# Kernel tuning notes

Hardware: AMD Instinct MI355X
Metric: run time of the kernel (lower is better)

The kernel has to match this reference:

```python
import jax, jax.numpy as jnp
import numpy as np

NEG_SLOPE = 0.2


def _gat(x, src, dst, W, a_src, a_dst, b, N):
    # PyG GATConv (eval mode, concat=True). W: [Fin, H*C], a_*: [H, C], b: [H*C]
    H, C = a_src.shape
    h = (x @ W).reshape(N, H, C)                       # [N,H,C]
    al_s = jnp.einsum('nhc,hc->nh', h, a_src)          # source attention logits
    al_d = jnp.einsum('nhc,hc->nh', h, a_dst)          # target attention logits
    e = jax.nn.leaky_relu(al_s[src] + al_d[dst], NEG_SLOPE)  # [E,H]
    m = jax.ops.segment_max(e, dst, num_segments=N)
    m = jnp.where(jnp.isneginf(m), 0.0, m)
    p = jnp.exp(e - m[dst])
    s = jax.ops.segment_sum(p, dst, num_segments=N)
    alpha = p / (s[dst] + 1e-16)                       # segment softmax over incoming edges
    out = jax.ops.segment_sum(h[src] * alpha[:, :, None], dst, num_segments=N)
    return out.reshape(N, H * C) + b


def _lin(key, fin, fout):
    k1, k2 = jax.random.split(key)
    w = jax.random.normal(k1, (fin, fout), jnp.float32) / np.sqrt(fin)
    b = jax.random.normal(k2, (fout,), jnp.float32) * 0.01
    return w, b


def _gat_params(key, fin, H, C):
    k1, k2, k3, k4 = jax.random.split(key, 4)
    W = jax.random.normal(k1, (fin, H * C), jnp.float32) / np.sqrt(fin)
    a_s = jax.random.normal(k2, (H, C), jnp.float32) / np.sqrt(C)
    a_d = jax.random.normal(k3, (H, C), jnp.float32) / np.sqrt(C)
    b = jax.random.normal(k4, (H * C,), jnp.float32) * 0.01
    return W, a_s, a_d, b


def setup_inputs() -> dict:
    key = jax.random.key(0)
    N, E, F, HID, H = 20000, 320000, 128, 128, 2
    W_ = HID * H  # 256
    ks = jax.random.split(key, 12)
    x = jax.random.normal(ks[0], (N, F), jnp.float32)
    edge_index = jax.random.randint(ks[1], (2, E), 0, N, jnp.int64)
    edge_attr = jax.random.normal(ks[2], (E, 4), jnp.float32)
    ec_w1, ec_b1 = _lin(ks[3], 2 * F, HID)
    ec_w2, ec_b2 = _lin(ks[4], HID, HID)
    g1 = _gat_params(ks[5], HID, H, HID)
    g2 = _gat_params(ks[6], W_, H, HID)
    reg_w, reg_b = _lin(ks[7], W_, W_)
    g3 = _gat_params(ks[8], W_, H, HID)
    g4 = _gat_params(ks[9], W_, H, HID)
    fin_w, fin_b = _lin(ks[10], W_, 1)
    d = {"x": x, "edge_index": edge_index, "edge_attr": edge_attr,
         "ec_w1": ec_w1, "ec_b1": ec_b1, "ec_w2": ec_w2, "ec_b2": ec_b2,
         "reg_w": reg_w, "reg_b": reg_b, "fin_w": fin_w, "fin_b": fin_b}
    for name, p in (("g1", g1), ("g2", g2), ("g3", g3), ("g4", g4)):
        d[name + "_w"], d[name + "_as"], d[name + "_ad"], d[name + "_b"] = p
    return d


def reference(x, edge_index, edge_attr,
              ec_w1, ec_b1, ec_w2, ec_b2,
              g1_w, g1_as, g1_ad, g1_b,
              g2_w, g2_as, g2_ad, g2_b,
              reg_w, reg_b,
              g3_w, g3_as, g3_ad, g3_b,
              g4_w, g4_as, g4_ad, g4_b,
              fin_w, fin_b):
    N = x.shape[0]
    src, dst = edge_index[0], edge_index[1]
    # EdgeConv: msg = MLP([x_i, x_j - x_i]), max-aggregation at target i (no self loops)
    xi = x[dst]
    msg = jnp.concatenate([xi, x[src] - xi], axis=-1)          # [E, 2F]
    h = jnp.maximum(msg @ ec_w1 + ec_b1, 0.0) @ ec_w2 + ec_b2   # [E, HID]
    agg = jax.ops.segment_max(h, dst, num_segments=N)
    x = jnp.where(jnp.isneginf(agg), 0.0, agg)
    # GATConv adds self loops by default
    loop = jnp.arange(N, dtype=src.dtype)
    s2 = jnp.concatenate([src, loop])
    d2 = jnp.concatenate([dst, loop])
    # edge_attr is ignored by GATConv (edge_dim=None)
    x = jax.nn.relu(_gat(x, s2, d2, g1_w, g1_as, g1_ad, g1_b, N))
    r = x
    x = jax.nn.relu(_gat(x, s2, d2, g2_w, g2_as, g2_ad, g2_b, N)) + r
    x = x @ reg_w + reg_b
    r = x
    x = jax.nn.relu(_gat(x, s2, d2, g3_w, g3_as, g3_ad, g3_b, N)) + r
    x = jax.nn.relu(_gat(x, s2, d2, g4_w, g4_as, g4_ad, g4_b, N))
    return x @ fin_w + fin_b
```

## Files before the change

kernel.cpp:

```cpp
#include <hip/hip_runtime.h>
#include <math.h>


#define NEG_SLOPE 0.2f

typedef short short8 __attribute__((ext_vector_type(8)));
typedef float float4v __attribute__((ext_vector_type(4)));

__device__ __forceinline__ float leaky(float x) { return x > 0.f ? x : NEG_SLOPE * x; }

__device__ __forceinline__ void atomicMaxF(float* addr, float v) {
  if (v >= 0.f) atomicMax((int*)addr, __float_as_int(v));
  else          atomicMin((unsigned int*)addr, __float_as_uint(v));
}

__device__ __forceinline__ unsigned short bf16_rn(float f) {
  unsigned u = __float_as_uint(f);
  unsigned r = (u + 0x7FFFu + ((u >> 16) & 1u)) >> 16;
  return (unsigned short)r;
}
__device__ __forceinline__ float bf16_to_f(unsigned short h) {
  return __uint_as_float(((unsigned)h) << 16);
}

__global__ __launch_bounds__(256) void k_fill_f32(float* p, float v, int n) {
  int i = blockIdx.x * 256 + threadIdx.x;
  if (i < n) p[i] = v;
}

__global__ __launch_bounds__(256) void k_hist(const int* __restrict__ ei, int* __restrict__ deg,
                                              int E) {
  int e = blockIdx.x * 256 + threadIdx.x;
  if (e < E) atomicAdd(&deg[ei[E + e]], 1);
}

__global__ __launch_bounds__(1024) void k_scan(const int* __restrict__ deg, int* __restrict__ rs,
                                               int n) {
  __shared__ int wsum[16];
  __shared__ int carry;
  int tid = threadIdx.x, lane = tid & 63, wv = tid >> 6;
  if (tid == 0) carry = 0;
  __syncthreads();
  for (int base = 0; base < n; base += 1024) {
    int i = base + tid;
    int v = (i < n) ? deg[i] : 0;
    int s = v;
    #pragma unroll
    for (int o = 1; o < 64; o <<= 1) {
      int t = __shfl(s, lane - o);
      if (lane >= o) s += t;
    }
    if (lane == 63) wsum[wv] = s;
    __syncthreads();
    if (wv == 0) {
      int x = (lane < 16) ? wsum[lane] : 0;
      #pragma unroll
      for (int o = 1; o < 16; o <<= 1) {
        int t = __shfl(x, lane - o);
        if (lane >= o) x += t;
      }
      if (lane < 16) wsum[lane] = x;
    }
    __syncthreads();
    int woff = carry + (wv ? wsum[wv - 1] : 0);
    if (i < n) rs[i] = woff + s - v;
    __syncthreads();
    if (tid == 0) carry += wsum[15];
    __syncthreads();
  }
  if (tid == 0) rs[n] = carry;
}

__global__ __launch_bounds__(256) void k_scatter(const int* __restrict__ ei,
                                                 const int* __restrict__ rs,
                                                 int* __restrict__ cnt,
                                                 int* __restrict__ csr_src,
                                                 int* __restrict__ csr_dst, int E) {
  int e = blockIdx.x * 256 + threadIdx.x;
  if (e < E) {
    int d = ei[E + e];
    int p = atomicAdd(&cnt[d], 1);
    int slot = rs[d] + p;
    csr_src[slot] = ei[e];
    csr_dst[slot] = d;
  }
}

struct SplitJob {
  const float* W;
  const float* aux;
  unsigned short* Th;
  unsigned short* Tl;
  float* bias_out;
  int K, N, kshift, type;
};
struct SplitJobs { SplitJob j[7]; };

__global__ __launch_bounds__(256) void k_prep_all(SplitJobs jobs) {
  SplitJob jb = jobs.j[blockIdx.y];
  int idx = blockIdx.x * 256 + threadIdx.x;
  if (idx >= jb.K * jb.N) return;
  float v;
  if (jb.type == 0) {
    int n = idx >> jb.kshift;
    int k = idx & (jb.K - 1);
    v = jb.W[k * jb.N + n];
  } else {
    int n = idx >> 7;
    int k = idx & 127;
    if (n < 128) v = jb.W[k * 128 + n] - jb.W[(k + 128) * 128 + n];
    else         v = jb.W[(k + 128) * 128 + (n - 128)];
    if (idx < 256) jb.bias_out[idx] = (idx < 128) ? jb.aux[idx] : 0.f;
  }
  unsigned short h = bf16_rn(v);
  jb.Th[idx] = h;
  jb.Tl[idx] = bf16_rn(v - bf16_to_f(h));
}

__global__ __launch_bounds__(256) void k_gemm_mfma(const float* __restrict__ A,
                                                   const unsigned short* __restrict__ BTh,
                                                   const unsigned short* __restrict__ BTl,
                                                   const float* __restrict__ bias,
                                                   float* __restrict__ C, int M, int K,
                                                   const float* __restrict__ a_s,
                                                   const float* __restrict__ a_d,
                                                   float* __restrict__ al_out) {
  __shared__ __align__(16) unsigned short Ash[64][40];
  __shared__ __align__(16) unsigned short Asl[64][40];
  __shared__ __align__(16) unsigned short Bsh[128][40];
  __shared__ __align__(16) unsigned short Bsl[128][40];
  __shared__ float alS[64][2];
  const int tid = threadIdx.x;
  const int bm = blockIdx.x * 64;
  const int bn = blockIdx.y * 128;
  const int w = tid >> 6, lane = tid & 63, quad = lane >> 4, lr = lane & 15;
  float4v zero4 = {0.f, 0.f, 0.f, 0.f};
  float4v acc[4][2];
  #pragma unroll
  for (int mt = 0; mt < 4; ++mt)
    #pragma unroll
    for (int nt = 0; nt < 2; ++nt) acc[mt][nt] = zero4;

  const int arow = tid >> 2;
  const int akq = (tid & 3) * 8;
  const int agr = bm + arow;

  #pragma unroll 4
  for (int k0 = 0; k0 < K; k0 += 32) {
    float av[8];
    if (agr < M) {
      float4 a0 = *(const float4*)&A[(size_t)agr * K + k0 + akq];
      float4 a1 = *(const float4*)&A[(size_t)agr * K + k0 + akq + 4];
      av[0] = a0.x; av[1] = a0.y; av[2] = a0.z; av[3] = a0.w;
      av[4] = a1.x; av[5] = a1.y; av[6] = a1.z; av[7] = a1.w;
    } else {
      #pragma unroll
      for (int i = 0; i < 8; ++i) av[i] = 0.f;
    }
    short8 h8, l8;
    #pragma unroll
    for (int i = 0; i < 8; ++i) {
      unsigned short h = bf16_rn(av[i]);
      h8[i] = (short)h;
      l8[i] = (short)bf16_rn(av[i] - bf16_to_f(h));
    }
    *(short8*)&Ash[arow][akq] = h8;
    *(short8*)&Asl[arow][akq] = l8;
    #pragma unroll
    for (int c = tid; c < 512; c += 256) {
      int n = c >> 2, kq2 = (c & 3) * 8;
      *(short8*)&Bsh[n][kq2] = *(const short8*)&BTh[(size_t)(bn + n) * K + k0 + kq2];
      *(short8*)&Bsl[n][kq2] = *(const short8*)&BTl[(size_t)(bn + n) * K + k0 + kq2];
    }
    __syncthreads();
    short8 ah[4], alo[4], bh[2], blo[2];
    #pragma unroll
    for (int mt = 0; mt < 4; ++mt) {
      ah[mt]  = *(short8*)&Ash[mt * 16 + lr][quad * 8];
      alo[mt] = *(short8*)&Asl[mt * 16 + lr][quad * 8];
    }
    #pragma unroll
    for (int nt = 0; nt < 2; ++nt) {
      bh[nt]  = *(short8*)&Bsh[w * 32 + nt * 16 + lr][quad * 8];
      blo[nt] = *(short8*)&Bsl[w * 32 + nt * 16 + lr][quad * 8];
    }
    #pragma unroll
    for (int mt = 0; mt < 4; ++mt)
      #pragma unroll
      for (int nt = 0; nt < 2; ++nt) {
        acc[mt][nt] = __builtin_amdgcn_mfma_f32_16x16x32_bf16(ah[mt], bh[nt], acc[mt][nt], 0, 0, 0);
        acc[mt][nt] = __builtin_amdgcn_mfma_f32_16x16x32_bf16(alo[mt], bh[nt], acc[mt][nt], 0, 0, 0);
        acc[mt][nt] = __builtin_amdgcn_mfma_f32_16x16x32_bf16(ah[mt], blo[nt], acc[mt][nt], 0, 0, 0);
      }
    __syncthreads();
  }
  #pragma unroll
  for (int nt = 0; nt < 2; ++nt) {
    int n = bn + w * 32 + nt * 16 + lr;
    float bv = bias ? bias[n] : 0.f;
    #pragma unroll
    for (int mt = 0; mt < 4; ++mt) {
      #pragma unroll
      for (int r = 0; r < 4; ++r) {
        int m = bm + mt * 16 + quad * 4 + r;
        if (m < M) C[(size_t)m * 256 + n] = acc[mt][nt][r] + bv;
      }
    }
  }
  if (a_s) {
    if (tid < 128) ((float*)alS)[tid] = 0.f;
    __syncthreads();
    float asv[2], adv[2];
    #pragma unroll
    for (int nt = 0; nt < 2; ++nt) {
      int n = bn + w * 32 + nt * 16 + lr;
      asv[nt] = a_s[n];
      adv[nt] = a_d[n];
    }
    #pragma unroll
    for (int mt = 0; mt < 4; ++mt) {
      #pragma unroll
      for (int r = 0; r < 4; ++r) {
        float ps = acc[mt][0][r] * asv[0] + acc[mt][1][r] * asv[1];
        float pd = acc[mt][0][r] * adv[0] + acc[mt][1][r] * adv[1];
        #pragma unroll
        for (int o = 8; o; o >>= 1) {
          ps += __shfl_xor(ps, o);
          pd += __shfl_xor(pd, o);
        }
        if (lr == 0) {
          int row = mt * 16 + quad * 4 + r;
          atomicAdd(&alS[row][0], ps);
          atomicAdd(&alS[row][1], pd);
        }
      }
    }
    __syncthreads();
    int head = bn >> 7;
    if (tid < 64) {
      int m = bm + tid;
      if (m < M) {
        al_out[m * 4 + head]     = alS[tid][0];
        al_out[m * 4 + 2 + head] = alS[tid][1];
      }
    }
  }
}

__global__ __launch_bounds__(256, 4) void k_edgeconv2(const float* __restrict__ uv,
                                                      const int* __restrict__ csr_src,
                                                      const int* __restrict__ csr_dst,
                                                      const unsigned short* __restrict__ w2Th,
                                                      const unsigned short* __restrict__ w2Tl,
                                                      const float* __restrict__ b2,
                                                      float* __restrict__ x0, int E) {
  __shared__ __align__(16) char smem[34816];
  unsigned short (*Ph)[136] = (unsigned short(*)[136])smem;
  unsigned short (*Pl)[136] = (unsigned short(*)[136])(smem + 17408);
  float (*H2)[132] = (float(*)[132])smem;
  __shared__ int sSrc[64], sDst[64];

  const int tid = threadIdx.x;
  const int e0 = blockIdx.x * 64;
  const int w = tid >> 6, lane = tid & 63, quad = lane >> 4, lr = lane & 15;
  if (tid < 64) {
    int e = e0 + tid;
    sSrc[tid] = (e < E) ? csr_src[e] : -1;
    sDst[tid] = (e < E) ? csr_dst[e] : -1;
  }
  __syncthreads();
  #pragma unroll
  for (int c = tid; c < 1024; c += 256) {
    int r = c >> 4;
    int kq = (c & 15) * 8;
    float pv[8];
    int sn = sSrc[r], dn = sDst[r];
    if (sn >= 0) {
      float4 u0 = *(const float4*)&uv[(size_t)dn * 256 + kq];
      float4 u1 = *(const float4*)&uv[(size_t)dn * 256 + kq + 4];
      float4 v0 = *(const float4*)&uv[(size_t)sn * 256 + 128 + kq];
      float4 v1 = *(const float4*)&uv[(size_t)sn * 256 + 128 + kq + 4];
      pv[0] = fmaxf(u0.x + v0.x, 0.f); pv[1] = fmaxf(u0.y + v0.y, 0.f);
      pv[2] = fmaxf(u0.z + v0.z, 0.f); pv[3] = fmaxf(u0.w + v0.w, 0.f);
      pv[4] = fmaxf(u1.x + v1.x, 0.f); pv[5] = fmaxf(u1.y + v1.y, 0.f);
      pv[6] = fmaxf(u1.z + v1.z, 0.f); pv[7] = fmaxf(u1.w + v1.w, 0.f);
    } else {
      #pragma unroll
      for (int i = 0; i < 8; ++i) pv[i] = 0.f;
    }
    short8 h8, l8;
    #pragma unroll
    for (int i = 0; i < 8; ++i) {
      unsigned short h = bf16_rn(pv[i]);
      h8[i] = (short)h;
      l8[i] = (short)bf16_rn(pv[i] - bf16_to_f(h));
    }
    *(short8*)&Ph[r][kq] = h8;
    *(short8*)&Pl[r][kq] = l8;
  }
  __syncthreads();
  float4v zero4 = {0.f, 0.f, 0.f, 0.f};
  float4v acc[4][2];
  #pragma unroll
  for (int mt = 0; mt < 4; ++mt)
    #pragma unroll
    for (int nt = 0; nt < 2; ++nt) acc[mt][nt] = zero4;

  #pragma unroll
  for (int k0 = 0; k0 < 128; k0 += 32) {
    short8 ah[4], alo[4], bh[2], blo[2];
    #pragma unroll
    for (int nt = 0; nt < 2; ++nt) {
      int n = w * 32 + nt * 16 + lr;
      bh[nt]  = *(const short8*)&w2Th[(size_t)n * 128 + k0 + quad * 8];
      blo[nt] = *(const short8*)&w2Tl[(size_t)n * 128 + k0 + quad * 8];
    }
    #pragma unroll
    for (int mt = 0; mt < 4; ++mt) {
      ah[mt]  = *(short8*)&Ph[mt * 16 + lr][k0 + quad * 8];
      alo[mt] = *(short8*)&Pl[mt * 16 + lr][k0 + quad * 8];
    }
    #pragma unroll
    for (int mt = 0; mt < 4; ++mt)
      #pragma unroll
      for (int nt = 0; nt < 2; ++nt) {
        acc[mt][nt] = __builtin_amdgcn_mfma_f32_16x16x32_bf16(ah[mt], bh[nt], acc[mt][nt], 0, 0, 0);
        acc[mt][nt] = __builtin_amdgcn_mfma_f32_16x16x32_bf16(alo[mt], bh[nt], acc[mt][nt], 0, 0, 0);
        acc[mt][nt] = __builtin_amdgcn_mfma_f32_16x16x32_bf16(ah[mt], blo[nt], acc[mt][nt], 0, 0, 0);
      }
  }
  __syncthreads();
  #pragma unroll
  for (int nt = 0; nt < 2; ++nt) {
    int n = w * 32 + nt * 16 + lr;
    float bv = b2[n];
    #pragma unroll
    for (int mt = 0; mt < 4; ++mt) {
      #pragma unroll
      for (int r = 0; r < 4; ++r) {
        int row = mt * 16 + quad * 4 + r;
        H2[row][n] = acc[mt][nt][r] + bv;
      }
    }
  }
  __syncthreads();
  if (tid < 128) {
    int col = tid;
    int prev = sDst[0];
    float rmax = H2[0][col];
    for (int r = 1; r < 64; ++r) {
      int d = sDst[r];
      float v = H2[r][col];
      if (d == prev) {
        rmax = fmaxf(rmax, v);
      } else {
        if (prev >= 0) atomicMaxF(&x0[(size_t)prev * 128 + col], rmax);
        prev = d;
        rmax = v;
      }
    }
    if (prev >= 0) atomicMaxF(&x0[(size_t)prev * 128 + col], rmax);
  }
}

__global__ __launch_bounds__(256) void k_finalize(float* p, int n) {
  int i = blockIdx.x * 256 + threadIdx.x;
  if (i < n) {
    float v = p[i];
    if (v == -INFINITY) p[i] = 0.f;
  }
}

__global__ __launch_bounds__(256) void k_gat_agg(const float* __restrict__ Hf,
                                                 const float* __restrict__ al,
                                                 const int* __restrict__ rs,
                                                 const int* __restrict__ csr_src,
                                                 const float* __restrict__ bias,
                                                 const float* __restrict__ res,
                                                 float* __restrict__ out, int N) {
  int wave = threadIdx.x >> 6, lane = threadIdx.x & 63;
  int i = blockIdx.x * 4 + wave;
  if (i >= N) return;
  int beg = rs[i], end = rs[i + 1];
  int deg = end - beg;
  float4 me = *(const float4*)&al[i * 4];
  float ad0 = me.z, ad1 = me.w;
  float sl0 = leaky(me.x + ad0);
  float sl1 = leaky(me.y + ad1);
  const int c = lane << 2;
  const int hsel = lane >> 5;
  float a0, a1, a2, a3;

  if (deg <= 64) {
    int s = 0;
    float l0 = -INFINITY, l1 = -INFINITY;
    bool act = lane < deg;
    if (act) {
      s = csr_src[beg + lane];
      float4 a4 = *(const float4*)&al[s * 4];
      l0 = leaky(a4.x + ad0);
      l1 = leaky(a4.y + ad1);
    }
    float m0 = fmaxf(sl0, l0), m1 = fmaxf(sl1, l1);
    #pragma unroll
    for (int o = 32; o; o >>= 1) {
      m0 = fmaxf(m0, __shfl_xor(m0, o));
      m1 = fmaxf(m1, __shfl_xor(m1, o));
    }
    float w0 = act ? __expf(l0 - m0) : 0.f;
    float w1 = act ? __expf(l1 - m1) : 0.f;
    float s0 = w0, s1 = w1;
    #pragma unroll
    for (int o = 32; o; o >>= 1) {
      s0 += __shfl_xor(s0, o);
      s1 += __shfl_xor(s1, o);
    }
    s0 += __expf(sl0 - m0);
    s1 += __expf(sl1 - m1);
    float inv0 = 1.f / (s0 + 1e-16f), inv1 = 1.f / (s1 + 1e-16f);
    float wp0 = w0 * inv0, wp1 = w1 * inv1;
    float wself = hsel ? __expf(sl1 - m1) * inv1 : __expf(sl0 - m0) * inv0;
    float4 hv = *(const float4*)&Hf[(size_t)i * 256 + c];
    a0 = wself * hv.x; a1 = wself * hv.y; a2 = wself * hv.z; a3 = wself * hv.w;
    float b0 = 0.f, b1 = 0.f, b2 = 0.f, b3 = 0.f;
    float c0 = 0.f, c1 = 0.f, c2 = 0.f, c3 = 0.f;
    float d0 = 0.f, d1 = 0.f, d2 = 0.f, d3 = 0.f;
    int j = 0;
    for (; j + 4 <= deg; j += 4) {
      int s_0 = __shfl(s, j);     float wA0 = __shfl(wp0, j);     float wB0 = __shfl(wp1, j);
      int s_1 = __shfl(s, j + 1); float wA1 = __shfl(wp0, j + 1); float wB1 = __shfl(wp1, j + 1);
      int s_2 = __shfl(s, j + 2); float wA2 = __shfl(wp0, j + 2); float wB2 = __shfl(wp1, j + 2);
      int s_3 = __shfl(s, j + 3); float wA3 = __shfl(wp0, j + 3); float wB3 = __shfl(wp1, j + 3);
      float4 h0 = *(const float4*)&Hf[(size_t)s_0 * 256 + c];
      float4 h1 = *(const float4*)&Hf[(size_t)s_1 * 256 + c];
      float4 h2 = *(const float4*)&Hf[(size_t)s_2 * 256 + c];
      float4 h3 = *(const float4*)&Hf[(size_t)s_3 * 256 + c];
      float w_0 = hsel ? wB0 : wA0;
      float w_1 = hsel ? wB1 : wA1;
      float w_2 = hsel ? wB2 : wA2;
      float w_3 = hsel ? wB3 : wA3;
      a0 += w_0 * h0.x; a1 += w_0 * h0.y; a2 += w_0 * h0.z; a3 += w_0 * h0.w;
      b0 += w_1 * h1.x; b1 += w_1 * h1.y; b2 += w_1 * h1.z; b3 += w_1 * h1.w;
      c0 += w_2 * h2.x; c1 += w_2 * h2.y; c2 += w_2 * h2.z; c3 += w_2 * h2.w;
      d0 += w_3 * h3.x; d1 += w_3 * h3.y; d2 += w_3 * h3.z; d3 += w_3 * h3.w;
    }
    for (; j < deg; ++j) {
      int sj = __shfl(s, j);
      float wA = __shfl(wp0, j), wB = __shfl(wp1, j);
      float wj = hsel ? wB : wA;
      float4 h4 = *(const float4*)&Hf[(size_t)sj * 256 + c];
      a0 += wj * h4.x; a1 += wj * h4.y; a2 += wj * h4.z; a3 += wj * h4.w;
    }
    a0 += b0 + c0 + d0; a1 += b1 + c1 + d1;
    a2 += b2 + c2 + d2; a3 += b3 + c3 + d3;
  } else {
    float m0 = sl0, m1 = sl1;
    for (int e = beg + lane; e < end; e += 64) {
      int s = csr_src[e];
      m0 = fmaxf(m0, leaky(al[s * 4 + 0] + ad0));
      m1 = fmaxf(m1, leaky(al[s * 4 + 1] + ad1));
    }
    #pragma unroll
    for (int o = 32; o; o >>= 1) {
      m0 = fmaxf(m0, __shfl_xor(m0, o));
      m1 = fmaxf(m1, __shfl_xor(m1, o));
    }
    float s0 = 0.f, s1 = 0.f;
    for (int e = beg + lane; e < end; e += 64) {
      int s = csr_src[e];
      s0 += __expf(leaky(al[s * 4 + 0] + ad0) - m0);
      s1 += __expf(leaky(al[s * 4 + 1] + ad1) - m1);
    }
    #pragma unroll
    for (int o = 32; o; o >>= 1) {
      s0 += __shfl_xor(s0, o);
      s1 += __shfl_xor(s1, o);
    }
    s0 += __expf(sl0 - m0);
    s1 += __expf(sl1 - m1);
    float inv0 = 1.f / (s0 + 1e-16f), inv1 = 1.f / (s1 + 1e-16f);
    float mh = hsel ? m1 : m0;
    float invh = hsel ? inv1 : inv0;
    float adh = hsel ? ad1 : ad0;
    float wself = __expf((hsel ? sl1 : sl0) - mh) * invh;
    float4 hv = *(const float4*)&Hf[(size_t)i * 256 + c];
    a0 = wself * hv.x; a1 = wself * hv.y; a2 = wself * hv.z; a3 = wself * hv.w;
    for (int e = beg; e < end; ++e) {
      int s = csr_src[e];
      float wgt = __expf(leaky(al[s * 4 + hsel] + adh) - mh) * invh;
      float4 h4 = *(const float4*)&Hf[(size_t)s * 256 + c];
      a0 += wgt * h4.x; a1 += wgt * h4.y; a2 += wgt * h4.z; a3 += wgt * h4.w;
    }
  }
  float4 bv = *(const float4*)&bias[c];
  float4 o4;
  o4.x = fmaxf(a0 + bv.x, 0.f);
  o4.y = fmaxf(a1 + bv.y, 0.f);
  o4.z = fmaxf(a2 + bv.z, 0.f);
  o4.w = fmaxf(a3 + bv.w, 0.f);
  if (res) {
    float4 r4 = *(const float4*)&res[(size_t)i * 256 + c];
    o4.x += r4.x; o4.y += r4.y; o4.z += r4.z; o4.w += r4.w;
  }
  *(float4*)&out[(size_t)i * 256 + c] = o4;
}

__global__ __launch_bounds__(256) void k_findot(const float* __restrict__ X,
                                                const float* __restrict__ fw,
                                                const float* __restrict__ fb,
                                                float* __restrict__ out, int N) {
  int wave = threadIdx.x >> 6, lane = threadIdx.x & 63;
  int i = blockIdx.x * 4 + wave;
  if (i >= N) return;
  float4 xv = *(const float4*)&X[(size_t)i * 256 + (lane << 2)];
  float4 wv = *(const float4*)&fw[lane << 2];
  float p = xv.x * wv.x + xv.y * wv.y + xv.z * wv.z + xv.w * wv.w;
  #pragma unroll
  for (int o = 32; o; o >>= 1) p += __shfl_xor(p, o);
  if (lane == 0) out[i] = p + fb[0];
}

extern "C" void kernel_launch(void* const* d_in, const int* in_sizes, int n_in,
                              void* d_out, int out_size, void* d_ws, size_t ws_size,
                              hipStream_t stream) {
  const float* x      = (const float*)d_in[0];
  const int*   ei     = (const int*)d_in[1];
  const float* ec_w1  = (const float*)d_in[3];
  const float* ec_b1  = (const float*)d_in[4];
  const float* ec_w2  = (const float*)d_in[5];
  const float* ec_b2  = (const float*)d_in[6];
  const float* reg_w  = (const float*)d_in[7];
  const float* reg_b  = (const float*)d_in[8];
  const float* fin_w  = (const float*)d_in[9];
  const float* fin_b  = (const float*)d_in[10];
  const float* g1_w   = (const float*)d_in[11];
  const float* g1_as  = (const float*)d_in[12];
  const float* g1_ad  = (const float*)d_in[13];
  const float* g1_b   = (const float*)d_in[14];
  const float* g2_w   = (const float*)d_in[15];
  const float* g2_as  = (const float*)d_in[16];
  const float* g2_ad  = (const float*)d_in[17];
  const float* g2_b   = (const float*)d_in[18];
  const float* g3_w   = (const float*)d_in[19];
  const float* g3_as  = (const float*)d_in[20];
  const float* g3_ad  = (const float*)d_in[21];
  const float* g3_b   = (const float*)d_in[22];
  const float* g4_w   = (const float*)d_in[23];
  const float* g4_as  = (const float*)d_in[24];
  const float* g4_ad  = (const float*)d_in[25];
  const float* g4_b   = (const float*)d_in[26];

  const int N = in_sizes[0] / 128;
  const int E = in_sizes[1] / 2;

  char* base = (char*)d_ws;
  size_t off = 0;
  auto alloc = [&](size_t bytes) -> char* {
    char* p = base + off;
    off += (bytes + 255) & ~(size_t)255;
    return p;
  };
  const size_t szN4 = ((size_t)N * 4 + 255) & ~(size_t)255;
  int*   deg      = (int*)alloc((size_t)N * 4);
  int*   cnt      = (int*)alloc((size_t)N * 4);
  int*   rs       = (int*)alloc((size_t)(N + 1) * 4);
  int*   csr_src  = (int*)alloc((size_t)E * 4);
  int*   csr_dst  = (int*)alloc((size_t)E * 4);
  float* bias_cat = (float*)alloc(256 * 4);
  unsigned short* bcatTh = (unsigned short*)alloc(256 * 128 * 2);
  unsigned short* bcatTl = (unsigned short*)alloc(256 * 128 * 2);
  unsigned short* w2Th   = (unsigned short*)alloc(128 * 128 * 2);
  unsigned short* w2Tl   = (unsigned short*)alloc(128 * 128 * 2);
  unsigned short* g1Th   = (unsigned short*)alloc(256 * 128 * 2);
  unsigned short* g1Tl   = (unsigned short*)alloc(256 * 128 * 2);
  unsigned short* g2Th   = (unsigned short*)alloc(256 * 256 * 2);
  unsigned short* g2Tl   = (unsigned short*)alloc(256 * 256 * 2);
  unsigned short* g3Th   = (unsigned short*)alloc(256 * 256 * 2);
  unsigned short* g3Tl   = (unsigned short*)alloc(256 * 256 * 2);
  unsigned short* g4Th   = (unsigned short*)alloc(256 * 256 * 2);
  unsigned short* g4Tl   = (unsigned short*)alloc(256 * 256 * 2);
  unsigned short* regTh  = (unsigned short*)alloc(256 * 256 * 2);
  unsigned short* regTl  = (unsigned short*)alloc(256 * 256 * 2);
  float* uv = (float*)alloc((size_t)N * 256 * 4);
  float* x0 = (float*)alloc((size_t)N * 128 * 4);
  float* X1 = (float*)alloc((size_t)N * 256 * 4);
  float* X2 = (float*)alloc((size_t)N * 256 * 4);
  float* al = (float*)alloc((size_t)N * 4 * 4);
  (void)ws_size; (void)n_in; (void)out_size;

  const int nodeWaveBlocks = (N + 3) / 4;
  const dim3 gemmGrid((N + 63) / 64, 2);

  SplitJobs jobs;
  jobs.j[0] = {ec_w2, nullptr, w2Th, w2Tl, nullptr, 128, 128, 7, 0};
  jobs.j[1] = {g1_w,  nullptr, g1Th, g1Tl, nullptr, 128, 256, 7, 0};
  jobs.j[2] = {g2_w,  nullptr, g2Th, g2Tl, nullptr, 256, 256, 8, 0};
  jobs.j[3] = {g3_w,  nullptr, g3Th, g3Tl, nullptr, 256, 256, 8, 0};
  jobs.j[4] = {g4_w,  nullptr, g4Th, g4Tl, nullptr, 256, 256, 8, 0};
  jobs.j[5] = {reg_w, nullptr, regTh, regTl, nullptr, 256, 256, 8, 0};
  jobs.j[6] = {ec_w1, ec_b1, bcatTh, bcatTl, bias_cat, 128, 256, 7, 1};
  k_prep_all<<<dim3(256, 7), 256, 0, stream>>>(jobs);

  hipMemsetAsync(deg, 0, 2 * szN4, stream);
  k_hist<<<(E + 255) / 256, 256, 0, stream>>>(ei, deg, E);
  k_scan<<<1, 1024, 0, stream>>>(deg, rs, N);
  k_scatter<<<(E + 255) / 256, 256, 0, stream>>>(ei, rs, cnt, csr_src, csr_dst, E);

  k_gemm_mfma<<<gemmGrid, 256, 0, stream>>>(x, bcatTh, bcatTl, bias_cat, uv, N, 128,
                                            nullptr, nullptr, nullptr);
  k_fill_f32<<<(N * 128 + 255) / 256, 256, 0, stream>>>(x0, -INFINITY, N * 128);
  k_edgeconv2<<<(E + 63) / 64, 256, 0, stream>>>(uv, csr_src, csr_dst, w2Th, w2Tl, ec_b2, x0, E);
  k_finalize<<<(N * 128 + 255) / 256, 256, 0, stream>>>(x0, N * 128);

  k_gemm_mfma<<<gemmGrid, 256, 0, stream>>>(x0, g1Th, g1Tl, nullptr, uv, N, 128,
                                            g1_as, g1_ad, al);
  k_gat_agg<<<nodeWaveBlocks, 256, 0, stream>>>(uv, al, rs, csr_src, g1_b, nullptr, X1, N);

  k_gemm_mfma<<<gemmGrid, 256, 0, stream>>>(X1, g2Th, g2Tl, nullptr, uv, N, 256,
                                            g2_as, g2_ad, al);
  k_gat_agg<<<nodeWaveBlocks, 256, 0, stream>>>(uv, al, rs, csr_src, g2_b, X1, X2, N);

  k_gemm_mfma<<<gemmGrid, 256, 0, stream>>>(X2, regTh, regTl, reg_b, X1, N, 256,
                                            nullptr, nullptr, nullptr);

  k_gemm_mfma<<<gemmGrid, 256, 0, stream>>>(X1, g3Th, g3Tl, nullptr, uv, N, 256,
                                            g3_as, g3_ad, al);
  k_gat_agg<<<nodeWaveBlocks, 256, 0, stream>>>(uv, al, rs, csr_src, g3_b, X1, X2, N);

  k_gemm_mfma<<<gemmGrid, 256, 0, stream>>>(X2, g4Th, g4Tl, nullptr, uv, N, 256,
                                            g4_as, g4_ad, al);
  k_gat_agg<<<nodeWaveBlocks, 256, 0, stream>>>(uv, al, rs, csr_src, g4_b, nullptr, X1, N);

  k_findot<<<nodeWaveBlocks, 256, 0, stream>>>(X1, fin_w, fin_b, (float*)d_out, N);
}
```

Baseline: 588.9 us.

## Pre-split activations to bf16 hi/lo in producers and drop GEMM LDS staging

Activations are now converted to bf16 high/low pairs once, in the producing kernel: the GAT aggregation epilogue, the GEMM epilogue, or a new split kernel. The -inf cleanup is folded into that split kernel, so the separate finalize launch goes away. The MFMA GEMM now loads A and B fragments straight from global memory, with no shared-memory staging and no barriers. This removes the per-tile fp32-to-bf16 split work and the synchronisation. In exchange, the four waves of a block load the same A rows redundantly and with less coalescing, and producers write extra hi/lo buffers.

```diff
diff --git a/kernel.cpp b/kernel.cpp
--- a/kernel.cpp
+++ b/kernel.cpp
@@ -6,6 +6,7 @@
 
 typedef short short8 __attribute__((ext_vector_type(8)));
 typedef float float4v __attribute__((ext_vector_type(4)));
+typedef unsigned short ushort4v __attribute__((ext_vector_type(4)));
 
 __device__ __forceinline__ float leaky(float x) { return x > 0.f ? x : NEG_SLOPE * x; }
 
@@ -26,6 +27,27 @@
 __global__ __launch_bounds__(256) void k_fill_f32(float* p, float v, int n) {
   int i = blockIdx.x * 256 + threadIdx.x;
   if (i < n) p[i] = v;
+}
+
+__global__ __launch_bounds__(256) void k_split_act(const float* __restrict__ src,
+                                                   unsigned short* __restrict__ h,
+                                                   unsigned short* __restrict__ l,
+                                                   int n, int fixinf) {
+  int i4 = (blockIdx.x * 256 + threadIdx.x) * 4;
+  if (i4 >= n) return;
+  float4 v = *(const float4*)&src[i4];
+  if (fixinf) {
+    if (v.x == -INFINITY) v.x = 0.f;
+    if (v.y == -INFINITY) v.y = 0.f;
+    if (v.z == -INFINITY) v.z = 0.f;
+    if (v.w == -INFINITY) v.w = 0.f;
+  }
+  unsigned short hx = bf16_rn(v.x), hy = bf16_rn(v.y), hz = bf16_rn(v.z), hw = bf16_rn(v.w);
+  ushort4v h4 = {hx, hy, hz, hw};
+  ushort4v l4 = {bf16_rn(v.x - bf16_to_f(hx)), bf16_rn(v.y - bf16_to_f(hy)),
+                 bf16_rn(v.z - bf16_to_f(hz)), bf16_rn(v.w - bf16_to_f(hw))};
+  *(ushort4v*)&h[i4] = h4;
+  *(ushort4v*)&l[i4] = l4;
 }
 
 __global__ __launch_bounds__(256) void k_hist(const int* __restrict__ ei, int* __restrict__ deg,
@@ -117,18 +139,17 @@
   jb.Tl[idx] = bf16_rn(v - bf16_to_f(h));
 }
 
-__global__ __launch_bounds__(256) void k_gemm_mfma(const float* __restrict__ A,
+__global__ __launch_bounds__(256) void k_gemm_mfma(const unsigned short* __restrict__ Ah,
+                                                   const unsigned short* __restrict__ Al,
                                                    const unsigned short* __restrict__ BTh,
                                                    const unsigned short* __restrict__ BTl,
                                                    const float* __restrict__ bias,
                                                    float* __restrict__ C, int M, int K,
+                                                   unsigned short* __restrict__ Ch,
+                                                   unsigned short* __restrict__ Cl,
                                                    const float* __restrict__ a_s,
                                                    const float* __restrict__ a_d,
                                                    float* __restrict__ al_out) {
-  __shared__ __align__(16) unsigned short Ash[64][40];
-  __shared__ __align__(16) unsigned short Asl[64][40];
-  __shared__ __align__(16) unsigned short Bsh[128][40];
-  __shared__ __align__(16) unsigned short Bsl[128][40];
   __shared__ float alS[64][2];
   const int tid = threadIdx.x;
   const int bm = blockIdx.x * 64;
@@ -141,48 +162,29 @@
     #pragma unroll
     for (int nt = 0; nt < 2; ++nt) acc[mt][nt] = zero4;
 
-  const int arow = tid >> 2;
-  const int akq = (tid & 3) * 8;
-  const int agr = bm + arow;
+  size_t aoff[4];
+  #pragma unroll
+  for (int mt = 0; mt < 4; ++mt) {
+    int m = bm + mt * 16 + lr;
+    aoff[mt] = (size_t)min(m, M - 1) * K;
+  }
+  size_t boff[2];
+  #pragma unroll
+  for (int nt = 0; nt < 2; ++nt) boff[nt] = (size_t)(bn + w * 32 + nt * 16 + lr) * K;
 
   #pragma unroll 4
   for (int k0 = 0; k0 < K; k0 += 32) {
-    float av[8];
-    if (agr < M) {
-      float4 a0 = *(const float4*)&A[(size_t)agr * K + k0 + akq];
-      float4 a1 = *(const float4*)&A[(size_t)agr * K + k0 + akq + 4];
-      av[0] = a0.x; av[1] = a0.y; av[2] = a0.z; av[3] = a0.w;
-      av[4] = a1.x; av[5] = a1.y; av[6] = a1.z; av[7] = a1.w;
-    } else {
-      #pragma unroll
-      for (int i = 0; i < 8; ++i) av[i] = 0.f;
-    }
-    short8 h8, l8;
-    #pragma unroll
-    for (int i = 0; i < 8; ++i) {
-      unsigned short h = bf16_rn(av[i]);
-      h8[i] = (short)h;
-      l8[i] = (short)bf16_rn(av[i] - bf16_to_f(h));
-    }
-    *(short8*)&Ash[arow][akq] = h8;
-    *(short8*)&Asl[arow][akq] = l8;
-    #pragma unroll
-    for (int c = tid; c < 512; c += 256) {
-      int n = c >> 2, kq2 = (c & 3) * 8;
-      *(short8*)&Bsh[n][kq2] = *(const short8*)&BTh[(size_t)(bn + n) * K + k0 + kq2];
-      *(short8*)&Bsl[n][kq2] = *(const short8*)&BTl[(size_t)(bn + n) * K + k0 + kq2];
-    }
-    __syncthreads();
+    const int kq = k0 + quad * 8;
     short8 ah[4], alo[4], bh[2], blo[2];
     #pragma unroll
     for (int mt = 0; mt < 4; ++mt) {
-      ah[mt]  = *(short8*)&Ash[mt * 16 + lr][quad * 8];
-      alo[mt] = *(short8*)&Asl[mt * 16 + lr][quad * 8];
+      ah[mt]  = *(const short8*)&Ah[aoff[mt] + kq];
+      alo[mt] = *(const short8*)&Al[aoff[mt] + kq];
     }
     #pragma unroll
     for (int nt = 0; nt < 2; ++nt) {
-      bh[nt]  = *(short8*)&Bsh[w * 32 + nt * 16 + lr][quad * 8];
-      blo[nt] = *(short8*)&Bsl[w * 32 + nt * 16 + lr][quad * 8];
+      bh[nt]  = *(const short8*)&BTh[boff[nt] + kq];
+      blo[nt] = *(const short8*)&BTl[boff[nt] + kq];
     }
     #pragma unroll
     for (int mt = 0; mt < 4; ++mt)
@@ -192,7 +194,6 @@
         acc[mt][nt] = __builtin_amdgcn_mfma_f32_16x16x32_bf16(alo[mt], bh[nt], acc[mt][nt], 0, 0, 0);
         acc[mt][nt] = __builtin_amdgcn_mfma_f32_16x16x32_bf16(ah[mt], blo[nt], acc[mt][nt], 0, 0, 0);
       }
-    __syncthreads();
   }
   #pragma unroll
   for (int nt = 0; nt < 2; ++nt) {
@@ -203,7 +204,16 @@
       #pragma unroll
       for (int r = 0; r < 4; ++r) {
         int m = bm + mt * 16 + quad * 4 + r;
-        if (m < M) C[(size_t)m * 256 + n] = acc[mt][nt][r] + bv;
+        if (m < M) {
+          float v = acc[mt][nt][r] + bv;
+          size_t idx = (size_t)m * 256 + n;
+          C[idx] = v;
+          if (Ch) {
+            unsigned short h = bf16_rn(v);
+            Ch[idx] = h;
+            Cl[idx] = bf16_rn(v - bf16_to_f(h));
+          }
+        }
       }
     }
   }
@@ -363,21 +373,15 @@
   }
 }
 
-__global__ __launch_bounds__(256) void k_finalize(float* p, int n) {
-  int i = blockIdx.x * 256 + threadIdx.x;
-  if (i < n) {
-    float v = p[i];
-    if (v == -INFINITY) p[i] = 0.f;
-  }
-}
-
 __global__ __launch_bounds__(256) void k_gat_agg(const float* __restrict__ Hf,
                                                  const float* __restrict__ al,
                                                  const int* __restrict__ rs,
                                                  const int* __restrict__ csr_src,
                                                  const float* __restrict__ bias,
                                                  const float* __restrict__ res,
-                                                 float* __restrict__ out, int N) {
+                                                 float* __restrict__ out,
+                                                 unsigned short* __restrict__ outh,
+                                                 unsigned short* __restrict__ outl, int N) {
   int wave = threadIdx.x >> 6, lane = threadIdx.x & 63;
   int i = blockIdx.x * 4 + wave;
   if (i >= N) return;
@@ -502,7 +506,16 @@
     float4 r4 = *(const float4*)&res[(size_t)i * 256 + c];
     o4.x += r4.x; o4.y += r4.y; o4.z += r4.z; o4.w += r4.w;
   }
-  *(float4*)&out[(size_t)i * 256 + c] = o4;
+  size_t idx = (size_t)i * 256 + c;
+  *(float4*)&out[idx] = o4;
+  if (outh) {
+    unsigned short hx = bf16_rn(o4.x), hy = bf16_rn(o4.y), hz = bf16_rn(o4.z), hw = bf16_rn(o4.w);
+    ushort4v h4 = {hx, hy, hz, hw};
+    ushort4v l4 = {bf16_rn(o4.x - bf16_to_f(hx)), bf16_rn(o4.y - bf16_to_f(hy)),
+                   bf16_rn(o4.z - bf16_to_f(hz)), bf16_rn(o4.w - bf16_to_f(hw))};
+    *(ushort4v*)&outh[idx] = h4;
+    *(ushort4v*)&outl[idx] = l4;
+  }
 }
 
 __global__ __launch_bounds__(256) void k_findot(const float* __restrict__ X,
@@ -586,10 +599,15 @@
   float* X1 = (float*)alloc((size_t)N * 256 * 4);
   float* X2 = (float*)alloc((size_t)N * 256 * 4);
   float* al = (float*)alloc((size_t)N * 4 * 4);
+  unsigned short* s1h = (unsigned short*)alloc((size_t)N * 256 * 2);
+  unsigned short* s1l = (unsigned short*)alloc((size_t)N * 256 * 2);
+  unsigned short* s2h = (unsigned short*)alloc((size_t)N * 256 * 2);
+  unsigned short* s2l = (unsigned short*)alloc((size_t)N * 256 * 2);
   (void)ws_size; (void)n_in; (void)out_size;
 
   const int nodeWaveBlocks = (N + 3) / 4;
   const dim3 gemmGrid((N + 63) / 64, 2);
+  const int splitBlocks128 = (N * 128 / 4 + 255) / 256;
 
   SplitJobs jobs;
   jobs.j[0] = {ec_w2, nullptr, w2Th, w2Tl, nullptr, 128, 128, 7, 0};
@@ -606,30 +624,35 @@
   k_scan<<<1, 1024, 0, stream>>>(deg, rs, N);
   k_scatter<<<(E + 255) / 256, 256, 0, stream>>>(ei, rs, cnt, csr_src, csr_dst, E);
 
-  k_gemm_mfma<<<gemmGrid, 256, 0, stream>>>(x, bcatTh, bcatTl, bias_cat, uv, N, 128,
-                                            nullptr, nullptr, nullptr);
+  k_split_act<<<splitBlocks128, 256, 0, stream>>>(x, s1h, s1l, N * 128, 0);
+  k_gemm_mfma<<<gemmGrid, 256, 0, stream>>>(s1h, s1l, bcatTh, bcatTl, bias_cat, uv, N, 128,
+                                            nullptr, nullptr, nullptr, nullptr, nullptr);
   k_fill_f32<<<(N * 128 + 255) / 256, 256, 0, stream>>>(x0, -INFINITY, N * 128);
   k_edgeconv2<<<(E + 63) / 64, 256, 0, stream>>>(uv, csr_src, csr_dst, w2Th, w2Tl, ec_b2, x0, E);
-  k_finalize<<<(N * 128 + 255) / 256, 256, 0, stream>>>(x0, N * 128);
-
-  k_gemm_mfma<<<gemmGrid, 256, 0, stream>>>(x0, g1Th, g1Tl, nullptr, uv, N, 128,
-                                            g1_as, g1_ad, al);
-  k_gat_agg<<<nodeWaveBlocks, 256, 0, stream>>>(uv, al, rs, csr_src, g1_b, nullptr, X1, N);
-
-  k_gemm_mfma<<<gemmGrid, 256, 0, stream>>>(X1, g2Th, g2Tl, nullptr, uv, N, 256,
-                                            g2_as, g2_ad, al);
-  k_gat_agg<<<nodeWaveBlocks, 256, 0, stream>>>(uv, al, rs, csr_src, g2_b, X1, X2, N);
-
-  k_gemm_mfma<<<gemmGrid, 256, 0, stream>>>(X2, regTh, regTl, reg_b, X1, N, 256,
-                                            nullptr, nullptr, nullptr);
-
-  k_gemm_mfma<<<gemmGrid, 256, 0, stream>>>(X1, g3Th, g3Tl, nullptr, uv, N, 256,
-                                            g3_as, g3_ad, al);
-  k_gat_agg<<<nodeWaveBlocks, 256, 0, stream>>>(uv, al, rs, csr_src, g3_b, X1, X2, N);
-
-  k_gemm_mfma<<<gemmGrid, 256, 0, stream>>>(X2, g4Th, g4Tl, nullptr, uv, N, 256,
-                                            g4_as, g4_ad, al);
-  k_gat_agg<<<nodeWaveBlocks, 256, 0, stream>>>(uv, al, rs, csr_src, g4_b, nullptr, X1, N);
+  k_split_act<<<splitBlocks128, 256, 0, stream>>>(x0, s1h, s1l, N * 128, 1);
+
+  k_gemm_mfma<<<gemmGrid, 256, 0, stream>>>(s1h, s1l, g1Th, g1Tl, nullptr, uv, N, 128,
+                                            nullptr, nullptr, g1_as, g1_ad, al);
+  k_gat_agg<<<nodeWaveBlocks, 256, 0, stream>>>(uv, al, rs, csr_src, g1_b, nullptr, X1,
+                                                s1h, s1l, N);
+
+  k_gemm_mfma<<<gemmGrid, 256, 0, stream>>>(s1h, s1l, g2Th, g2Tl, nullptr, uv, N, 256,
+                                            nullptr, nullptr, g2_as, g2_ad, al);
+  k_gat_agg<<<nodeWaveBlocks, 256, 0, stream>>>(uv, al, rs, csr_src, g2_b, X1, X2,
+                                                s2h, s2l, N);
+
+  k_gemm_mfma<<<gemmGrid, 256, 0, stream>>>(s2h, s2l, regTh, regTl, reg_b, X1, N, 256,
+                                            s1h, s1l, nullptr, nullptr, nullptr);
+
+  k_gemm_mfma<<<gemmGrid, 256, 0, stream>>>(s1h, s1l, g3Th, g3Tl, nullptr, uv, N, 256,
+                                            nullptr, nullptr, g3_as, g3_ad, al);
+  k_gat_agg<<<nodeWaveBlocks, 256, 0, stream>>>(uv, al, rs, csr_src, g3_b, X1, X2,
+                                                s2h, s2l, N);
+
+  k_gemm_mfma<<<gemmGrid, 256, 0, stream>>>(s2h, s2l, g4Th, g4Tl, nullptr, uv, N, 256,
+                                            nullptr, nullptr, g4_as, g4_ad, al);
+  k_gat_agg<<<nodeWaveBlocks, 256, 0, stream>>>(uv, al, rs, csr_src, g4_b, nullptr, X1,
+                                                nullptr, nullptr, N);
 
   k_findot<<<nodeWaveBlocks, 256, 0, stream>>>(X1, fin_w, fin_b, (float*)d_out, N);
 }
```

Result: slower. 695.8 us (+18.2%).
